# Kernel optimization log

Measured on AMD Instinct MI355X. Metric: run time of the kernel, lower is better.

Reference implementation:

```python
import jax, jax.numpy as jnp
import numpy as np

C = 128      # block channels
K = 7        # involution kernel size
GC = 16      # group_ch
G = (C // 2) // GC  # involution groups = 4


def conv1x1(x, w, b):
    # x: (B,Cin,H,W), w: (Cout,Cin)
    return jnp.einsum('bchw,oc->bohw', x, w) + b[None, :, None, None]


def conv2d(x, w, b, pad):
    y = jax.lax.conv_general_dilated(
        x, w, window_strides=(1, 1), padding=((pad, pad), (pad, pad)),
        dimension_numbers=('NCHW', 'OIHW', 'NCHW'))
    return y + b[None, :, None, None]


def prelu(x, a):
    return jnp.where(x >= 0, x, a * x)


def patches7(x):
    # x: (B,C,H,W) -> (B,C,K*K,H,W), same padding (torch Unfold, pad=3)
    B, Cc, H, W = x.shape
    p = K // 2
    xp = jnp.pad(x, ((0, 0), (0, 0), (p, p), (p, p)))
    return jnp.stack([xp[:, :, i:i + H, j:j + W]
                      for i in range(K) for j in range(K)], axis=2)


def setup_inputs() -> dict:
    key = jax.random.key(0)
    ks = jax.random.split(key, 9)
    f32 = jnp.float32
    def w(k, shape, s=0.02):
        return jax.random.normal(k, shape, f32) * s
    d = {}
    d['x'] = jax.random.normal(ks[0], (2, C, 128, 128), f32)
    # conv1: C -> C//2, 1x1
    d['w1'] = w(ks[1], (C // 2, C)); d['b1'] = jnp.zeros((C // 2,), f32)
    d['a1'] = jnp.float32(0.25)  # PReLU (single param)
    # involution reduce: C//2 -> C//4, 1x1 (+ReLU)
    d['wr'] = w(ks[2], (C // 4, C // 2)); d['br'] = jnp.zeros((C // 4,), f32)
    # involution span: C//4 -> G*K*K, 1x1
    d['ws'] = w(ks[3], (G * K * K, C // 4)); d['bs'] = jnp.zeros((G * K * K,), f32)
    d['a2'] = jnp.float32(0.25)
    # conv2: C//2 -> C, 1x1
    d['w2'] = w(ks[4], (C, C // 2)); d['b2'] = jnp.zeros((C,), f32)
    # attn conv: 2 -> 1, 7x7 pad 3
    d['wa'] = w(ks[5], (1, 2, 7, 7)); d['ba'] = jnp.zeros((1,), f32)
    # psec: 3x3 (C//4->C//4) + PReLU + 1x1 (C//4->C)
    d['wp1'] = w(ks[6], (C // 4, C // 4, 3, 3)); d['bp1'] = jnp.zeros((C // 4,), f32)
    d['ap'] = jnp.float32(0.25)
    d['wp2'] = w(ks[7], (C, C // 4)); d['bp2'] = jnp.zeros((C,), f32)
    return d


def reference(x, w1, b1, a1, wr, br, ws, bs, a2, w2, b2, wa, ba, wp1, bp1, ap, wp2, bp2):
    B, _, H, W = x.shape
    x1 = prelu(conv1x1(x, w1, b1), a1)                       # (B, C/2, H, W)
    # involution: per-pixel dynamic kernels
    f = jax.nn.relu(conv1x1(x1, wr, br))                     # (B, C/4, H, W)
    kw = conv1x1(f, ws, bs).reshape(B, G, 1, K * K, H, W)    # dynamic kernels
    pat = patches7(x1).reshape(B, G, GC, K * K, H, W)        # unfolded patches
    x2 = (kw * pat).sum(axis=3).reshape(B, C // 2, H, W)     # multiply-reduce
    x3 = conv1x1(prelu(x2, a2), w2, b2)                      # (B, C, H, W)
    # attention gate on f (ZPool -> 7x7 conv -> sigmoid)
    zp = jnp.concatenate([f.max(axis=1, keepdims=True),
                          f.mean(axis=1, keepdims=True)], axis=1)
    attn = jax.nn.sigmoid(conv2d(zp, wa, ba, 3))             # (B, 1, H, W)
    x4 = x3 * attn
    ps = conv1x1(prelu(conv2d(f, wp1, bp1, 1), ap), wp2, bp2)
    return x4 + ps
```

## Files before the change

### kernel.cpp

```cpp
#include <hip/hip_runtime.h>

#define HW_  16384
#define NPX  32768

__device__ __forceinline__ float prelu_(float x, float a) { return x >= 0.f ? x : a * x; }

__global__ __launch_bounds__(256, 3) void k_front(const float* __restrict__ x,
        const float* __restrict__ w1, const float* __restrict__ b1,
        const float* __restrict__ a1p, const float* __restrict__ wr,
        const float* __restrict__ br, float* __restrict__ x1,
        float* __restrict__ f, float* __restrict__ zp) {
    __shared__ float sA[12544];
    float* xs  = sA;
    float* wT1 = sA + 4096;
    int p0 = blockIdx.x << 6;
    int b = p0 >> 14, hw0 = p0 & 16383;

    for (int e = threadIdx.x; e < 8192; e += 256) {
        int o = e >> 7, c = e & 127;
        wT1[o * 132 + c] = w1[e];
    }
    int pq = threadIdx.x & 15;
    int og = threadIdx.x >> 4;
    const float a1 = a1p[0];
    float4 acc[4];
    #pragma unroll
    for (int u = 0; u < 4; ++u) { float bv = b1[og * 4 + u]; acc[u] = make_float4(bv, bv, bv, bv); }
    const float* xb = x + (b << 21) + hw0;
    #pragma unroll 1
    for (int half = 0; half < 2; ++half) {
        float4 xv[4];
        #pragma unroll
        for (int i = 0; i < 4; ++i) {
            int e = threadIdx.x + (i << 8);
            xv[i] = *(const float4*)&xb[((half * 64 + (e >> 4)) << 14) + ((e & 15) << 2)];
        }
        __syncthreads();
        #pragma unroll
        for (int i = 0; i < 4; ++i) {
            int e = threadIdx.x + (i << 8);
            *(float4*)&xs[((e >> 4) << 6) + ((e & 15) << 2)] = xv[i];
        }
        __syncthreads();
        #pragma unroll 4
        for (int c4 = 0; c4 < 16; ++c4) {
            float4 taps[4];
            #pragma unroll
            for (int j = 0; j < 4; ++j)
                taps[j] = *(const float4*)&xs[((c4 * 4 + j) << 6) + (pq << 2)];
            #pragma unroll
            for (int u = 0; u < 4; ++u) {
                float4 wv = *(const float4*)&wT1[(og * 4 + u) * 132 + half * 64 + c4 * 4];
                acc[u].x = fmaf(wv.x, taps[0].x, acc[u].x); acc[u].y = fmaf(wv.x, taps[0].y, acc[u].y);
                acc[u].z = fmaf(wv.x, taps[0].z, acc[u].z); acc[u].w = fmaf(wv.x, taps[0].w, acc[u].w);
                acc[u].x = fmaf(wv.y, taps[1].x, acc[u].x); acc[u].y = fmaf(wv.y, taps[1].y, acc[u].y);
                acc[u].z = fmaf(wv.y, taps[1].z, acc[u].z); acc[u].w = fmaf(wv.y, taps[1].w, acc[u].w);
                acc[u].x = fmaf(wv.z, taps[2].x, acc[u].x); acc[u].y = fmaf(wv.z, taps[2].y, acc[u].y);
                acc[u].z = fmaf(wv.z, taps[2].z, acc[u].z); acc[u].w = fmaf(wv.z, taps[2].w, acc[u].w);
                acc[u].x = fmaf(wv.w, taps[3].x, acc[u].x); acc[u].y = fmaf(wv.w, taps[3].y, acc[u].y);
                acc[u].z = fmaf(wv.w, taps[3].z, acc[u].z); acc[u].w = fmaf(wv.w, taps[3].w, acc[u].w);
            }
        }
    }
    float4 res[4];
    #pragma unroll
    for (int u = 0; u < 4; ++u) {
        res[u].x = prelu_(acc[u].x, a1); res[u].y = prelu_(acc[u].y, a1);
        res[u].z = prelu_(acc[u].z, a1); res[u].w = prelu_(acc[u].w, a1);
        *(float4*)(x1 + ((b * 64 + og * 4 + u) << 14) + hw0 + (pq << 2)) = res[u];
    }
    __syncthreads();
    float* x1t = sA;
    float* wrT = sA + 4352;
    float* ft  = sA + 6432;
    #pragma unroll
    for (int u = 0; u < 4; ++u)
        *(float4*)&x1t[(og * 4 + u) * 68 + (pq << 2)] = res[u];
    for (int e = threadIdx.x; e < 2048; e += 256) {
        int fo = e >> 6, c = e & 63;
        wrT[fo * 65 + c] = wr[e];
    }
    __syncthreads();
    int pq2 = threadIdx.x & 15;
    int fg = threadIdx.x >> 4;
    float4 fa[2];
    #pragma unroll
    for (int u = 0; u < 2; ++u) { float bv = br[fg * 2 + u]; fa[u] = make_float4(bv, bv, bv, bv); }
    #pragma unroll 4
    for (int c = 0; c < 64; ++c) {
        float4 tap = *(const float4*)&x1t[c * 68 + (pq2 << 2)];
        #pragma unroll
        for (int u = 0; u < 2; ++u) {
            float wv = wrT[(fg * 2 + u) * 65 + c];
            fa[u].x = fmaf(wv, tap.x, fa[u].x);
            fa[u].y = fmaf(wv, tap.y, fa[u].y);
            fa[u].z = fmaf(wv, tap.z, fa[u].z);
            fa[u].w = fmaf(wv, tap.w, fa[u].w);
        }
    }
    #pragma unroll
    for (int u = 0; u < 2; ++u) {
        float4 r;
        r.x = fmaxf(fa[u].x, 0.f); r.y = fmaxf(fa[u].y, 0.f);
        r.z = fmaxf(fa[u].z, 0.f); r.w = fmaxf(fa[u].w, 0.f);
        *(float4*)(f + ((b * 32 + fg * 2 + u) << 14) + hw0 + (pq2 << 2)) = r;
        *(float4*)&ft[(fg * 2 + u) * 68 + (pq2 << 2)] = r;
    }
    __syncthreads();
    if (threadIdx.x < 64) {
        int px = threadIdx.x;
        float mx = ft[px], sm = ft[px];
        #pragma unroll
        for (int c = 1; c < 32; ++c) {
            float v = ft[c * 68 + px];
            mx = fmaxf(mx, v); sm += v;
        }
        zp[((b * 2 + 0) << 14) + hw0 + px] = mx;
        zp[((b * 2 + 1) << 14) + hw0 + px] = sm * (1.f / 32.f);
    }
}

__global__ __launch_bounds__(256, 4) void k_mid2(const float* __restrict__ x1,
        const float* __restrict__ f, const float* __restrict__ ws_,
        const float* __restrict__ bs, float* __restrict__ x2,
        const float* __restrict__ zp, const float* __restrict__ wp1,
        const float* __restrict__ bp1, const float* __restrict__ app,
        float* __restrict__ p1, const float* __restrict__ wa,
        const float* __restrict__ ba, float* __restrict__ attn) {
    __shared__ float smem[8448];
    if (blockIdx.x < 512) {
        float* tile = smem;
        int g = blockIdx.x >> 7;
        int t = blockIdx.x & 127;
        int b = t >> 6;
        int th = (t >> 3) & 7, tw = t & 7;
        int h0 = th * 16, w0 = tw * 16;
        const float* x1g = x1 + ((b * 64 + g * 16) << 14);
        #pragma unroll 1
        for (int rem = threadIdx.x; rem < 484; rem += 256) {
            int r = rem / 22, cl = rem - r * 22;
            int hh = h0 + r - 3, ww = w0 + cl - 3;
            bool ok = (hh >= 0 && hh < 128 && ww >= 0 && ww < 128);
            const float* src = x1g + (hh << 7) + ww;
            float v[16];
            #pragma unroll
            for (int c = 0; c < 16; ++c) v[c] = ok ? src[c << 14] : 0.f;
            float* dst = tile + r * 24 + cl;
            #pragma unroll
            for (int c = 0; c < 16; ++c) dst[c * 528] = v[c];
        }
        int lh = threadIdx.x >> 4, lw = threadIdx.x & 15;
        int hw = ((h0 + lh) << 7) + w0 + lw;
        float fv[32];
        const float* fp = f + (b << 19) + hw;
        #pragma unroll
        for (int c = 0; c < 32; ++c) fv[c] = fp[c << 14];
        __syncthreads();
        float acc[16];
        #pragma unroll
        for (int u = 0; u < 16; ++u) acc[u] = 0.f;
        const float* tap0 = tile + lh * 24 + lw;
        const float* wk = ws_ + g * 49 * 32;
        const float* bsg = bs + g * 49;
        #pragma unroll 1
        for (int di = 0; di < 7; ++di) {
            #pragma unroll 1
            for (int dj = 0; dj < 7; ++dj) {
                int kk = di * 7 + dj;
                float kwv = bsg[kk];
                const float* wkk = wk + kk * 32;
                #pragma unroll
                for (int c = 0; c < 32; ++c) kwv = fmaf(wkk[c], fv[c], kwv);
                const float* tp = tap0 + di * 24 + dj;
                #pragma unroll
                for (int u = 0; u < 16; ++u)
                    acc[u] = fmaf(kwv, tp[u * 528], acc[u]);
            }
        }
        float* op = x2 + ((b * 64 + g * 16) << 14) + hw;
        #pragma unroll
        for (int u = 0; u < 16; ++u) op[u << 14] = acc[u];
    } else if (blockIdx.x < 1024) {
        float* fs = smem;
        float* wT = smem + 6080;
        int bid = blockIdx.x - 512;
        int half = bid >> 8;
        int t = bid & 255;
        int b = t >> 7;
        int tl = t & 127;
        int th = tl >> 3, tw = tl & 7;
        int h0 = th * 8, w0 = tw * 16;
        int o0 = half * 16;
        const float* fb = f + (b << 19);
        #pragma unroll 1
        for (int rem = threadIdx.x; rem < 180; rem += 256) {
            int r = rem / 18, cl = rem - r * 18;
            int hh = h0 + r - 1, ww = w0 + cl - 1;
            bool ok = (hh >= 0 && hh < 128 && ww >= 0 && ww < 128);
            const float* src = fb + (hh << 7) + ww;
            float* dst = fs + r * 19 + cl;
            #pragma unroll 1
            for (int cb = 0; cb < 4; ++cb) {
                float v[8];
                #pragma unroll
                for (int c = 0; c < 8; ++c) v[c] = ok ? src[(cb * 8 + c) << 14] : 0.f;
                #pragma unroll
                for (int c = 0; c < 8; ++c) dst[(cb * 8 + c) * 190] = v[c];
            }
        }
        int pxq = threadIdx.x & 31;
        int rowq = pxq >> 2, colq = pxq & 3;
        int oh = threadIdx.x >> 5;
        const float ap = app[0];
        float acc[2][4];
        #pragma unroll
        for (int o = 0; o < 2; ++o) {
            float bv = bp1[o0 + oh * 2 + o];
            #pragma unroll
            for (int px = 0; px < 4; ++px) acc[o][px] = bv;
        }
        const float* fsb = fs + rowq * 19 + colq * 4;
        #pragma unroll 1
        for (int cih = 0; cih < 2; ++cih) {
            __syncthreads();
            #pragma unroll 1
            for (int e = threadIdx.x; e < 2304; e += 256) {
                int o = e / 144, i = e - o * 144;
                wT[o * 145 + i] = wp1[(o0 + o) * 288 + cih * 144 + i];
            }
            __syncthreads();
            #pragma unroll 1
            for (int cl_ = 0; cl_ < 16; ++cl_) {
                int ci = cih * 16 + cl_;
                float tap[3][6];
                const float* base = fsb + ci * 190;
                #pragma unroll
                for (int r = 0; r < 3; ++r)
                    #pragma unroll
                    for (int j = 0; j < 6; ++j)
                        tap[r][j] = base[r * 19 + j];
                #pragma unroll
                for (int ki = 0; ki < 3; ++ki)
                    #pragma unroll
                    for (int kj = 0; kj < 3; ++kj) {
                        int idx = cl_ * 9 + ki * 3 + kj;
                        float w0v = wT[(oh * 2 + 0) * 145 + idx];
                        float w1v = wT[(oh * 2 + 1) * 145 + idx];
                        #pragma unroll
                        for (int px = 0; px < 4; ++px) {
                            float tv = tap[ki][px + kj];
                            acc[0][px] = fmaf(w0v, tv, acc[0][px]);
                            acc[1][px] = fmaf(w1v, tv, acc[1][px]);
                        }
                    }
            }
        }
        int hw = ((h0 + rowq) << 7) + w0 + colq * 4;
        #pragma unroll
        for (int o = 0; o < 2; ++o) {
            float4 r;
            r.x = prelu_(acc[o][0], ap); r.y = prelu_(acc[o][1], ap);
            r.z = prelu_(acc[o][2], ap); r.w = prelu_(acc[o][3], ap);
            *(float4*)(p1 + ((b * 32 + o0 + oh * 2 + o) << 14) + hw) = r;
        }
    } else {
        float* zs = smem;
        int t = blockIdx.x - 1024;
        int b = t >> 6;
        int tile = t & 63;
        int th = tile >> 3, tw = tile & 7;
        int h0 = th * 16, w0 = tw * 16;
        const float* zb = zp + (b << 15);
        #pragma unroll 1
        for (int rem = threadIdx.x; rem < 484; rem += 256) {
            int r = rem / 22, cl = rem - r * 22;
            int hh = h0 + r - 3, ww = w0 + cl - 3;
            bool ok = (hh >= 0 && hh < 128 && ww >= 0 && ww < 128);
            const float* src = zb + (hh << 7) + ww;
            float v0 = ok ? src[0] : 0.f;
            float v1 = ok ? src[HW_] : 0.f;
            zs[r * 23 + cl] = v0;
            zs[506 + r * 23 + cl] = v1;
        }
        __syncthreads();
        int lh = threadIdx.x >> 4, lw = threadIdx.x & 15;
        float acc = ba[0];
        #pragma unroll
        for (int c = 0; c < 2; ++c) {
            const float* zc = &zs[c * 506 + lh * 23 + lw];
            #pragma unroll
            for (int i = 0; i < 7; ++i)
                #pragma unroll
                for (int j = 0; j < 7; ++j)
                    acc = fmaf(wa[c * 49 + i * 7 + j], zc[i * 23 + j], acc);
        }
        attn[(b << 14) + ((h0 + lh) << 7) + w0 + lw] = 1.f / (1.f + expf(-acc));
    }
}

__global__ __launch_bounds__(256, 2) void k_final(const float* __restrict__ x2,
        const float* __restrict__ p1, const float* __restrict__ attn,
        const float* __restrict__ a2p, const float* __restrict__ w2,
        const float* __restrict__ b2, const float* __restrict__ wp2,
        const float* __restrict__ bp2, float* __restrict__ out) {
    __shared__ float xs2[64 * 128];
    __shared__ float ps[32 * 128];
    __shared__ float wT2[64 * 36];
    __shared__ float wTp[32 * 36];
    __shared__ float as_[128];
    int split = blockIdx.x >> 8;
    int tile = blockIdx.x & 255;
    int b = tile >> 7;
    int hw0 = (tile & 127) << 7;
    int o0 = split * 32;
    const float a2 = a2p[0];

    for (int e = threadIdx.x; e < 2048; e += 256) {
        int o = e >> 6, c = e & 63;
        wT2[c * 36 + o] = w2[(o0 + o) * 64 + c];
    }
    for (int e = threadIdx.x; e < 1024; e += 256) {
        int o = e >> 5, c = e & 31;
        wTp[c * 36 + o] = wp2[(o0 + o) * 32 + c];
    }
    {
        const float4* xb = (const float4*)(x2 + (b << 20) + hw0);
        float4 xv[8];
        #pragma unroll
        for (int i = 0; i < 8; ++i) {
            int e = threadIdx.x + i * 256;
            xv[i] = xb[((e >> 5) << 12) + (e & 31)];
        }
        #pragma unroll
        for (int i = 0; i < 8; ++i) {
            int e = threadIdx.x + i * 256;
            float4 v = xv[i];
            v.x = prelu_(v.x, a2); v.y = prelu_(v.y, a2);
            v.z = prelu_(v.z, a2); v.w = prelu_(v.w, a2);
            *(float4*)&xs2[(e >> 5) * 128 + (e & 31) * 4] = v;
        }
        const float4* pb = (const float4*)(p1 + (b << 19) + hw0);
        float4 pv[4];
        #pragma unroll
        for (int i = 0; i < 4; ++i) {
            int e = threadIdx.x + i * 256;
            pv[i] = pb[((e >> 5) << 12) + (e & 31)];
        }
        #pragma unroll
        for (int i = 0; i < 4; ++i) {
            int e = threadIdx.x + i * 256;
            *(float4*)&ps[(e >> 5) * 128 + (e & 31) * 4] = pv[i];
        }
        if (threadIdx.x < 32)
            ((float4*)as_)[threadIdx.x] = ((const float4*)(attn + (b << 14) + hw0))[threadIdx.x];
    }
    int pr = threadIdx.x & 63;
    int og = threadIdx.x >> 6;
    float b2v[8], bpv[8];
    #pragma unroll
    for (int u = 0; u < 8; ++u) { b2v[u] = b2[o0 + og * 8 + u]; bpv[u] = bp2[o0 + og * 8 + u]; }
    __syncthreads();

    float2 acc[8];
    #pragma unroll
    for (int u = 0; u < 8; ++u) acc[u] = make_float2(0.f, 0.f);
    #pragma unroll 8
    for (int c = 0; c < 64; ++c) {
        float2 tap = *(const float2*)&xs2[c * 128 + pr * 2];
        const float* wb = &wT2[c * 36 + og * 8];
        float4 wva = *(const float4*)wb;
        float4 wvb = *(const float4*)(wb + 4);
        acc[0].x = fmaf(wva.x, tap.x, acc[0].x); acc[0].y = fmaf(wva.x, tap.y, acc[0].y);
        acc[1].x = fmaf(wva.y, tap.x, acc[1].x); acc[1].y = fmaf(wva.y, tap.y, acc[1].y);
        acc[2].x = fmaf(wva.z, tap.x, acc[2].x); acc[2].y = fmaf(wva.z, tap.y, acc[2].y);
        acc[3].x = fmaf(wva.w, tap.x, acc[3].x); acc[3].y = fmaf(wva.w, tap.y, acc[3].y);
        acc[4].x = fmaf(wvb.x, tap.x, acc[4].x); acc[4].y = fmaf(wvb.x, tap.y, acc[4].y);
        acc[5].x = fmaf(wvb.y, tap.x, acc[5].x); acc[5].y = fmaf(wvb.y, tap.y, acc[5].y);
        acc[6].x = fmaf(wvb.z, tap.x, acc[6].x); acc[6].y = fmaf(wvb.z, tap.y, acc[6].y);
        acc[7].x = fmaf(wvb.w, tap.x, acc[7].x); acc[7].y = fmaf(wvb.w, tap.y, acc[7].y);
    }
    float2 at = *(const float2*)&as_[pr * 2];
    #pragma unroll
    for (int u = 0; u < 8; ++u) {
        acc[u].x = (acc[u].x + b2v[u]) * at.x + bpv[u];
        acc[u].y = (acc[u].y + b2v[u]) * at.y + bpv[u];
    }
    #pragma unroll 8
    for (int c = 0; c < 32; ++c) {
        float2 tap = *(const float2*)&ps[c * 128 + pr * 2];
        const float* wb = &wTp[c * 36 + og * 8];
        float4 wva = *(const float4*)wb;
        float4 wvb = *(const float4*)(wb + 4);
        acc[0].x = fmaf(wva.x, tap.x, acc[0].x); acc[0].y = fmaf(wva.x, tap.y, acc[0].y);
        acc[1].x = fmaf(wva.y, tap.x, acc[1].x); acc[1].y = fmaf(wva.y, tap.y, acc[1].y);
        acc[2].x = fmaf(wva.z, tap.x, acc[2].x); acc[2].y = fmaf(wva.z, tap.y, acc[2].y);
        acc[3].x = fmaf(wva.w, tap.x, acc[3].x); acc[3].y = fmaf(wva.w, tap.y, acc[3].y);
        acc[4].x = fmaf(wvb.x, tap.x, acc[4].x); acc[4].y = fmaf(wvb.x, tap.y, acc[4].y);
        acc[5].x = fmaf(wvb.y, tap.x, acc[5].x); acc[5].y = fmaf(wvb.y, tap.y, acc[5].y);
        acc[6].x = fmaf(wvb.z, tap.x, acc[6].x); acc[6].y = fmaf(wvb.z, tap.y, acc[6].y);
        acc[7].x = fmaf(wvb.w, tap.x, acc[7].x); acc[7].y = fmaf(wvb.w, tap.y, acc[7].y);
    }
    #pragma unroll
    for (int u = 0; u < 8; ++u)
        *(float2*)(out + ((b * 128 + o0 + og * 8 + u) << 14) + hw0 + pr * 2) = acc[u];
}

extern "C" void kernel_launch(void* const* d_in, const int* in_sizes, int n_in,
                              void* d_out, int out_size, void* d_ws, size_t ws_size,
                              hipStream_t stream) {
    const float* x   = (const float*)d_in[0];
    const float* w1  = (const float*)d_in[1];
    const float* b1  = (const float*)d_in[2];
    const float* a1  = (const float*)d_in[3];
    const float* wr  = (const float*)d_in[4];
    const float* br  = (const float*)d_in[5];
    const float* ws_ = (const float*)d_in[6];
    const float* bs  = (const float*)d_in[7];
    const float* a2  = (const float*)d_in[8];
    const float* w2  = (const float*)d_in[9];
    const float* b2  = (const float*)d_in[10];
    const float* wa  = (const float*)d_in[11];
    const float* ba  = (const float*)d_in[12];
    const float* wp1 = (const float*)d_in[13];
    const float* bp1 = (const float*)d_in[14];
    const float* ap  = (const float*)d_in[15];
    const float* wp2 = (const float*)d_in[16];
    const float* bp2 = (const float*)d_in[17];
    float* out = (float*)d_out;

    float* w = (float*)d_ws;
    float* ws_x1   = w;
    float* ws_f    = ws_x1 + 2 * 64 * HW_;
    float* ws_x2   = ws_f  + 2 * 32 * HW_;
    float* ws_zp   = ws_x2 + 2 * 64 * HW_;
    float* ws_attn = ws_zp + 2 * 2 * HW_;
    float* ws_p1   = ws_attn + NPX;

    hipLaunchKernelGGL(k_front, dim3(512), dim3(256), 0, stream,
                       x, w1, b1, a1, wr, br, ws_x1, ws_f, ws_zp);
    hipLaunchKernelGGL(k_mid2, dim3(1152), dim3(256), 0, stream,
                       ws_x1, ws_f, ws_, bs, ws_x2, ws_zp,
                       wp1, bp1, ap, ws_p1, wa, ba, ws_attn);
    hipLaunchKernelGGL(k_final, dim3(1024), dim3(256), 0, stream,
                       ws_x2, ws_p1, ws_attn, a2, w2, b2, wp2, bp2, out);
}
```

Before: 176.3 us.

## Stream activations directly from global in final 1x1 conv and fold PReLU upstream

The PReLU on the involution output now runs in the mid kernel's store epilogue, so the final kernel reads pre-activated values. The final kernel drops its shared-memory staging of x2, p1 and attn. Each thread instead loads float4 pixel vectors straight from global memory in channel chunks of 8 and computes 4 output channels by 4 pixels, with 16 output channels per block. Smaller shared memory allows occupancy 4 instead of 2, but each pixel tile is now re-read from global once per output split (8 splits instead of 4), raising global or L2 traffic.

```diff
diff --git a/kernel.cpp b/kernel.cpp
--- a/kernel.cpp
+++ b/kernel.cpp
@@ -126,7 +126,8 @@
         const float* __restrict__ zp, const float* __restrict__ wp1,
         const float* __restrict__ bp1, const float* __restrict__ app,
         float* __restrict__ p1, const float* __restrict__ wa,
-        const float* __restrict__ ba, float* __restrict__ attn) {
+        const float* __restrict__ ba, float* __restrict__ attn,
+        const float* __restrict__ a2p) {
     __shared__ float smem[8448];
     if (blockIdx.x < 512) {
         float* tile = smem;
@@ -177,9 +178,10 @@
                     acc[u] = fmaf(kwv, tp[u * 528], acc[u]);
             }
         }
+        const float a2 = a2p[0];
         float* op = x2 + ((b * 64 + g * 16) << 14) + hw;
         #pragma unroll
-        for (int u = 0; u < 16; ++u) op[u << 14] = acc[u];
+        for (int u = 0; u < 16; ++u) op[u << 14] = prelu_(acc[u], a2);
     } else if (blockIdx.x < 1024) {
         float* fs = smem;
         float* wT = smem + 6080;
@@ -298,111 +300,86 @@
     }
 }
 
-__global__ __launch_bounds__(256, 2) void k_final(const float* __restrict__ x2,
+__global__ __launch_bounds__(256, 4) void k_final(const float* __restrict__ x2p,
         const float* __restrict__ p1, const float* __restrict__ attn,
-        const float* __restrict__ a2p, const float* __restrict__ w2,
-        const float* __restrict__ b2, const float* __restrict__ wp2,
-        const float* __restrict__ bp2, float* __restrict__ out) {
-    __shared__ float xs2[64 * 128];
-    __shared__ float ps[32 * 128];
-    __shared__ float wT2[64 * 36];
-    __shared__ float wTp[32 * 36];
-    __shared__ float as_[128];
-    int split = blockIdx.x >> 8;
-    int tile = blockIdx.x & 255;
-    int b = tile >> 7;
-    int hw0 = (tile & 127) << 7;
-    int o0 = split * 32;
-    const float a2 = a2p[0];
-
-    for (int e = threadIdx.x; e < 2048; e += 256) {
-        int o = e >> 6, c = e & 63;
-        wT2[c * 36 + o] = w2[(o0 + o) * 64 + c];
-    }
+        const float* __restrict__ w2, const float* __restrict__ b2,
+        const float* __restrict__ wp2, const float* __restrict__ bp2,
+        float* __restrict__ out) {
+    __shared__ float wT2[64 * 20];
+    __shared__ float wTp[32 * 20];
+    int split = blockIdx.x >> 7;
+    int tile = blockIdx.x & 127;
+    int p0 = tile << 8;
+    int b = p0 >> 14, hw0 = p0 & 16383;
+    int o0 = split * 16;
+
     for (int e = threadIdx.x; e < 1024; e += 256) {
-        int o = e >> 5, c = e & 31;
-        wTp[c * 36 + o] = wp2[(o0 + o) * 32 + c];
-    }
-    {
-        const float4* xb = (const float4*)(x2 + (b << 20) + hw0);
+        int o = e & 15, c = e >> 4;
+        wT2[c * 20 + o] = w2[(o0 + o) * 64 + c];
+    }
+    for (int e = threadIdx.x; e < 512; e += 256) {
+        int o = e & 15, c = e >> 4;
+        wTp[c * 20 + o] = wp2[(o0 + o) * 32 + c];
+    }
+    int q4 = threadIdx.x & 63;
+    int og = threadIdx.x >> 6;
+    float b2v[4], bpv[4];
+    #pragma unroll
+    for (int u = 0; u < 4; ++u) { b2v[u] = b2[o0 + og * 4 + u]; bpv[u] = bp2[o0 + og * 4 + u]; }
+    float4 acc[4];
+    #pragma unroll
+    for (int u = 0; u < 4; ++u) acc[u] = make_float4(0.f, 0.f, 0.f, 0.f);
+    __syncthreads();
+
+    const float* xb = x2p + (b << 20) + hw0 + (q4 << 2);
+    #pragma unroll 1
+    for (int cb = 0; cb < 8; ++cb) {
         float4 xv[8];
         #pragma unroll
-        for (int i = 0; i < 8; ++i) {
-            int e = threadIdx.x + i * 256;
-            xv[i] = xb[((e >> 5) << 12) + (e & 31)];
-        }
-        #pragma unroll
-        for (int i = 0; i < 8; ++i) {
-            int e = threadIdx.x + i * 256;
-            float4 v = xv[i];
-            v.x = prelu_(v.x, a2); v.y = prelu_(v.y, a2);
-            v.z = prelu_(v.z, a2); v.w = prelu_(v.w, a2);
-            *(float4*)&xs2[(e >> 5) * 128 + (e & 31) * 4] = v;
-        }
-        const float4* pb = (const float4*)(p1 + (b << 19) + hw0);
-        float4 pv[4];
-        #pragma unroll
-        for (int i = 0; i < 4; ++i) {
-            int e = threadIdx.x + i * 256;
-            pv[i] = pb[((e >> 5) << 12) + (e & 31)];
-        }
-        #pragma unroll
-        for (int i = 0; i < 4; ++i) {
-            int e = threadIdx.x + i * 256;
-            *(float4*)&ps[(e >> 5) * 128 + (e & 31) * 4] = pv[i];
-        }
-        if (threadIdx.x < 32)
-            ((float4*)as_)[threadIdx.x] = ((const float4*)(attn + (b << 14) + hw0))[threadIdx.x];
-    }
-    int pr = threadIdx.x & 63;
-    int og = threadIdx.x >> 6;
-    float b2v[8], bpv[8];
-    #pragma unroll
-    for (int u = 0; u < 8; ++u) { b2v[u] = b2[o0 + og * 8 + u]; bpv[u] = bp2[o0 + og * 8 + u]; }
-    __syncthreads();
-
-    float2 acc[8];
-    #pragma unroll
-    for (int u = 0; u < 8; ++u) acc[u] = make_float2(0.f, 0.f);
-    #pragma unroll 8
-    for (int c = 0; c < 64; ++c) {
-        float2 tap = *(const float2*)&xs2[c * 128 + pr * 2];
-        const float* wb = &wT2[c * 36 + og * 8];
-        float4 wva = *(const float4*)wb;
-        float4 wvb = *(const float4*)(wb + 4);
-        acc[0].x = fmaf(wva.x, tap.x, acc[0].x); acc[0].y = fmaf(wva.x, tap.y, acc[0].y);
-        acc[1].x = fmaf(wva.y, tap.x, acc[1].x); acc[1].y = fmaf(wva.y, tap.y, acc[1].y);
-        acc[2].x = fmaf(wva.z, tap.x, acc[2].x); acc[2].y = fmaf(wva.z, tap.y, acc[2].y);
-        acc[3].x = fmaf(wva.w, tap.x, acc[3].x); acc[3].y = fmaf(wva.w, tap.y, acc[3].y);
-        acc[4].x = fmaf(wvb.x, tap.x, acc[4].x); acc[4].y = fmaf(wvb.x, tap.y, acc[4].y);
-        acc[5].x = fmaf(wvb.y, tap.x, acc[5].x); acc[5].y = fmaf(wvb.y, tap.y, acc[5].y);
-        acc[6].x = fmaf(wvb.z, tap.x, acc[6].x); acc[6].y = fmaf(wvb.z, tap.y, acc[6].y);
-        acc[7].x = fmaf(wvb.w, tap.x, acc[7].x); acc[7].y = fmaf(wvb.w, tap.y, acc[7].y);
-    }
-    float2 at = *(const float2*)&as_[pr * 2];
-    #pragma unroll
-    for (int u = 0; u < 8; ++u) {
+        for (int j = 0; j < 8; ++j) xv[j] = *(const float4*)&xb[(cb * 8 + j) << 14];
+        #pragma unroll
+        for (int j = 0; j < 8; ++j) {
+            float4 wv = *(const float4*)&wT2[(cb * 8 + j) * 20 + og * 4];
+            acc[0].x = fmaf(wv.x, xv[j].x, acc[0].x); acc[0].y = fmaf(wv.x, xv[j].y, acc[0].y);
+            acc[0].z = fmaf(wv.x, xv[j].z, acc[0].z); acc[0].w = fmaf(wv.x, xv[j].w, acc[0].w);
+            acc[1].x = fmaf(wv.y, xv[j].x, acc[1].x); acc[1].y = fmaf(wv.y, xv[j].y, acc[1].y);
+            acc[1].z = fmaf(wv.y, xv[j].z, acc[1].z); acc[1].w = fmaf(wv.y, xv[j].w, acc[1].w);
+            acc[2].x = fmaf(wv.z, xv[j].x, acc[2].x); acc[2].y = fmaf(wv.z, xv[j].y, acc[2].y);
+            acc[2].z = fmaf(wv.z, xv[j].z, acc[2].z); acc[2].w = fmaf(wv.z, xv[j].w, acc[2].w);
+            acc[3].x = fmaf(wv.w, xv[j].x, acc[3].x); acc[3].y = fmaf(wv.w, xv[j].y, acc[3].y);
+            acc[3].z = fmaf(wv.w, xv[j].z, acc[3].z); acc[3].w = fmaf(wv.w, xv[j].w, acc[3].w);
+        }
+    }
+    float4 at = *(const float4*)(attn + (b << 14) + hw0 + (q4 << 2));
+    #pragma unroll
+    for (int u = 0; u < 4; ++u) {
         acc[u].x = (acc[u].x + b2v[u]) * at.x + bpv[u];
         acc[u].y = (acc[u].y + b2v[u]) * at.y + bpv[u];
-    }
-    #pragma unroll 8
-    for (int c = 0; c < 32; ++c) {
-        float2 tap = *(const float2*)&ps[c * 128 + pr * 2];
-        const float* wb = &wTp[c * 36 + og * 8];
-        float4 wva = *(const float4*)wb;
-        float4 wvb = *(const float4*)(wb + 4);
-        acc[0].x = fmaf(wva.x, tap.x, acc[0].x); acc[0].y = fmaf(wva.x, tap.y, acc[0].y);
-        acc[1].x = fmaf(wva.y, tap.x, acc[1].x); acc[1].y = fmaf(wva.y, tap.y, acc[1].y);
-        acc[2].x = fmaf(wva.z, tap.x, acc[2].x); acc[2].y = fmaf(wva.z, tap.y, acc[2].y);
-        acc[3].x = fmaf(wva.w, tap.x, acc[3].x); acc[3].y = fmaf(wva.w, tap.y, acc[3].y);
-        acc[4].x = fmaf(wvb.x, tap.x, acc[4].x); acc[4].y = fmaf(wvb.x, tap.y, acc[4].y);
-        acc[5].x = fmaf(wvb.y, tap.x, acc[5].x); acc[5].y = fmaf(wvb.y, tap.y, acc[5].y);
-        acc[6].x = fmaf(wvb.z, tap.x, acc[6].x); acc[6].y = fmaf(wvb.z, tap.y, acc[6].y);
-        acc[7].x = fmaf(wvb.w, tap.x, acc[7].x); acc[7].y = fmaf(wvb.w, tap.y, acc[7].y);
-    }
-    #pragma unroll
-    for (int u = 0; u < 8; ++u)
-        *(float2*)(out + ((b * 128 + o0 + og * 8 + u) << 14) + hw0 + pr * 2) = acc[u];
+        acc[u].z = (acc[u].z + b2v[u]) * at.z + bpv[u];
+        acc[u].w = (acc[u].w + b2v[u]) * at.w + bpv[u];
+    }
+    const float* pb = p1 + (b << 19) + hw0 + (q4 << 2);
+    #pragma unroll 1
+    for (int cb = 0; cb < 4; ++cb) {
+        float4 pv[8];
+        #pragma unroll
+        for (int j = 0; j < 8; ++j) pv[j] = *(const float4*)&pb[(cb * 8 + j) << 14];
+        #pragma unroll
+        for (int j = 0; j < 8; ++j) {
+            float4 wv = *(const float4*)&wTp[(cb * 8 + j) * 20 + og * 4];
+            acc[0].x = fmaf(wv.x, pv[j].x, acc[0].x); acc[0].y = fmaf(wv.x, pv[j].y, acc[0].y);
+            acc[0].z = fmaf(wv.x, pv[j].z, acc[0].z); acc[0].w = fmaf(wv.x, pv[j].w, acc[0].w);
+            acc[1].x = fmaf(wv.y, pv[j].x, acc[1].x); acc[1].y = fmaf(wv.y, pv[j].y, acc[1].y);
+            acc[1].z = fmaf(wv.y, pv[j].z, acc[1].z); acc[1].w = fmaf(wv.y, pv[j].w, acc[1].w);
+            acc[2].x = fmaf(wv.z, pv[j].x, acc[2].x); acc[2].y = fmaf(wv.z, pv[j].y, acc[2].y);
+            acc[2].z = fmaf(wv.z, pv[j].z, acc[2].z); acc[2].w = fmaf(wv.z, pv[j].w, acc[2].w);
+            acc[3].x = fmaf(wv.w, pv[j].x, acc[3].x); acc[3].y = fmaf(wv.w, pv[j].y, acc[3].y);
+            acc[3].z = fmaf(wv.w, pv[j].z, acc[3].z); acc[3].w = fmaf(wv.w, pv[j].w, acc[3].w);
+        }
+    }
+    #pragma unroll
+    for (int u = 0; u < 4; ++u)
+        *(float4*)(out + ((b * 128 + o0 + og * 4 + u) << 14) + hw0 + (q4 << 2)) = acc[u];
 }
 
 extern "C" void kernel_launch(void* const* d_in, const int* in_sizes, int n_in,
@@ -440,7 +417,7 @@
                        x, w1, b1, a1, wr, br, ws_x1, ws_f, ws_zp);
     hipLaunchKernelGGL(k_mid2, dim3(1152), dim3(256), 0, stream,
                        ws_x1, ws_f, ws_, bs, ws_x2, ws_zp,
-                       wp1, bp1, ap, ws_p1, wa, ba, ws_attn);
+                       wp1, bp1, ap, ws_p1, wa, ba, ws_attn, a2);
     hipLaunchKernelGGL(k_final, dim3(1024), dim3(256), 0, stream,
-                       ws_x2, ws_p1, ws_attn, a2, w2, b2, wp2, bp2, out);
+                       ws_x2, ws_p1, ws_attn, w2, b2, wp2, bp2, out);
 }
```

Measured after the change: 174.5 us (median of 2 runs). Within noise of the previous version (-1.0%).
